# Performance work log

Measured on AMD Instinct MI355X. Metric: run time of the kernel, lower is better.

Reference implementation:

```python
import jax, jax.numpy as jnp
import numpy as np

M_USERS = 100000
N_ITEMS = 50000
N_NODES = M_USERS + N_ITEMS
DIM = 64
N_INTER = 1600000
BATCH = 16384
N_NEG = 40
REG = 1e-4


def setup_inputs() -> dict:
    key = jax.random.key(0)
    ks = jax.random.split(key, 12)
    xavier = lambda k, shape: jax.random.normal(k, shape, jnp.float32) * np.sqrt(2.0 / (shape[-1] + shape[-2] if len(shape) >= 2 else shape[-1] + 1))
    E = jax.random.normal(ks[0], (N_NODES, DIM), jnp.float32) * 0.1
    E2 = jax.random.normal(ks[1], (N_NODES, DIM), jnp.float32) * 0.1
    Wm = jax.random.normal(ks[2], (2, DIM, DIM), jnp.float32) * np.sqrt(1.0 / DIM)
    bm = jnp.zeros((2, DIM), jnp.float32)
    attn_W = jax.random.normal(ks[3], (DIM, DIM), jnp.float32) * np.sqrt(1.0 / DIM)
    attn_b = jnp.zeros((DIM,), jnp.float32)
    q_w = jax.random.normal(ks[4], (DIM,), jnp.float32) * np.sqrt(1.0 / DIM)
    # symmetric bipartite edge list: users in [0, M), items in [M, M+N)
    eu = jax.random.randint(ks[5], (N_INTER,), 0, M_USERS, jnp.int32)
    ei = jax.random.randint(ks[6], (N_INTER,), M_USERS, N_NODES, jnp.int32)
    edge_index = jnp.stack([jnp.concatenate([eu, ei]), jnp.concatenate([ei, eu])], axis=0)
    u = jax.random.randint(ks[7], (BATCH,), 0, M_USERS, jnp.int32)
    v = jax.random.randint(ks[8], (BATCH,), M_USERS, N_NODES, jnp.int32)
    n = jax.random.randint(ks[9], (BATCH, N_NEG), M_USERS, N_NODES, jnp.int32)
    w = jax.random.uniform(ks[10], (BATCH,), jnp.float32, 0.5, 5.0)  # ratings; only sign() used
    return {"E": E, "E2": E2, "Wm": Wm, "bm": bm, "attn_W": attn_W, "attn_b": attn_b,
            "q_w": q_w, "edge_index": edge_index, "u": u, "v": v, "n": n, "w": w}


def _lightgconv(x, src, dst, norm):
    # out[i] = sum_{(j->i)} norm_e * x[j]   (symmetric-normalized LightGCN propagate)
    msg = x[src] * norm[:, None]  # [E, D]
    return jax.ops.segment_sum(msg, dst, num_segments=N_NODES)


def _aggregate(E, E2, Wm, bm, attn_W, attn_b, q_w, edge_index):
    src, dst = edge_index[0], edge_index[1]
    deg = jax.ops.segment_sum(jnp.ones(src.shape, E.dtype), dst, num_segments=N_NODES)
    dinv = jnp.where(deg > 0, jax.lax.rsqrt(jnp.maximum(deg, 1.0)), 0.0)
    norm = dinv[src] * dinv[dst]
    # GNN branch: B = [E, conv(E), conv(conv(E))]; z_p = mean
    b1 = _lightgconv(E, src, dst, norm)
    b2 = _lightgconv(b1, src, dst, norm)
    z_p = (E + b1 + b2) / 3.0
    # MLP branch (eval mode: dropout disabled); z_n is output of last MLP layer
    x = jax.nn.relu(E2 @ Wm[0].T + bm[0])
    x = jax.nn.relu(x @ Wm[1].T + bm[1])
    z_n = x
    # attention fusion
    w_p = jnp.tanh(z_p @ attn_W.T + attn_b) @ q_w  # [Nn]
    w_n = jnp.tanh(z_n @ attn_W.T + attn_b) @ q_w  # [Nn]
    alpha = jax.nn.softmax(jnp.stack([w_p, w_n], axis=1), axis=1)  # [Nn, 2]
    return alpha[:, 0:1] * z_p + alpha[:, 1:2] * z_n


def reference(E, E2, Wm, bm, attn_W, attn_b, q_w, edge_index, u, v, n, w):
    Z = _aggregate(E, E2, Wm, bm, attn_W, attn_b, q_w, edge_index)
    u_ = Z[u]            # [B, D]
    v_ = Z[v]            # [B, D]
    n_ = Z[n]            # [B, K, D]
    pos = jnp.sum(u_ * v_, axis=1)                      # [B]
    neg = jnp.einsum('bd,bkd->bk', u_, n_)              # [B, K]
    sbpr = jax.nn.log_sigmoid(jnp.sign(w)[:, None] * pos[:, None] - neg).sum(axis=1)
    reg_loss = jnp.sum(u_ ** 2) + jnp.sum(v_ ** 2) + jnp.sum(n_ ** 2)
    return -jnp.sum(sbpr) + REG * reg_loss
```

## Files before the change

### kernel.cpp

```cpp
#include <hip/hip_runtime.h>
#include <math.h>


typedef unsigned int uint;
typedef unsigned short ushort;
typedef unsigned long long ull;
typedef __attribute__((ext_vector_type(8))) short short8v;
typedef __attribute__((ext_vector_type(4))) float float4v;
typedef __attribute__((ext_vector_type(2))) float float2v;

#define BK_SHIFT 9
#define BK_SIZE 512
#define CAP 20480

#if __has_builtin(__builtin_amdgcn_cvt_pk_f32_fp8) && __has_builtin(__builtin_amdgcn_cvt_pk_fp8_f32)
#define HW_FP8 1
#else
#define HW_FP8 0
#endif

__device__ inline float b2f(ushort u) { return __uint_as_float(((uint)u) << 16); }
__device__ inline ushort f2b(float f) {
  uint u = __float_as_uint(f);
  return (ushort)((u + 0x7fffu + ((u >> 16) & 1u)) >> 16);
}
__device__ inline uint pack2(float lo, float hi) {
  return (uint)f2b(lo) | ((uint)f2b(hi) << 16);
}

__device__ inline float dec1(uint u) {
  uint e = (u >> 3) & 0xFu;
  uint m = u & 7u;
  uint s = (u & 0x80u) << 24;
  float norm = __uint_as_float(s | ((e + 120u) << 23) | (m << 20));
  float den = __uint_as_float(s | 0x3F800000u) * (float)(int)m * 0.001953125f;
  return e ? norm : den;
}
__device__ inline uint enc1(float x) {
  uint s = (__float_as_uint(x) >> 24) & 0x80u;
  float ax = fminf(fabsf(x), 448.f);
  uint r;
  if (ax < 0.015625f) {
    r = (uint)(int)rintf(ax * 512.f);
  } else {
    uint b = __float_as_uint(ax);
    b += 0x7FFFFu + ((b >> 20) & 1u);
    uint e = (b >> 23) - 120u;
    r = (e > 15u) ? 0x7Eu : ((e << 3) | ((b >> 20) & 7u));
  }
  return s | r;
}
__device__ inline float4 dec4(uint v) {
#if HW_FP8
  float2v lo = __builtin_amdgcn_cvt_pk_f32_fp8((int)v, false);
  float2v hi = __builtin_amdgcn_cvt_pk_f32_fp8((int)v, true);
  return make_float4(lo[0], lo[1], hi[0], hi[1]);
#else
  return make_float4(dec1(v & 0xFFu), dec1((v >> 8) & 0xFFu),
                     dec1((v >> 16) & 0xFFu), dec1(v >> 24));
#endif
}
__device__ inline uint enc4f(float a, float b, float c, float d) {
#if HW_FP8
  int v = 0;
  v = __builtin_amdgcn_cvt_pk_fp8_f32(a, b, v, false);
  v = __builtin_amdgcn_cvt_pk_fp8_f32(c, d, v, true);
  return (uint)v;
#else
  return enc1(a) | (enc1(b) << 8) | (enc1(c) << 16) | (enc1(d) << 24);
#endif
}

__global__ void k_half(const float* __restrict__ x, ushort* __restrict__ out, int n8) {
  int i = blockIdx.x * blockDim.x + threadIdx.x;
  if (i >= n8) return;
  const float4* p = (const float4*)(x + (size_t)i * 8);
  float4 a = p[0], b = p[1];
  uint4 o;
  o.x = pack2(a.x, a.y); o.y = pack2(a.z, a.w);
  o.z = pack2(b.x, b.y); o.w = pack2(b.z, b.w);
  ((uint4*)out)[i] = o;
}

__global__ void k_conv_e(const float* __restrict__ x, uint* __restrict__ out8,
                         ushort* __restrict__ outh, int n16) {
  int i = blockIdx.x * blockDim.x + threadIdx.x;
  if (i >= n16) return;
  const float4* p = (const float4*)(x + (size_t)i * 16);
  float4 f0 = p[0], f1 = p[1], f2 = p[2], f3 = p[3];
  uint4 o8;
  o8.x = enc4f(f0.x, f0.y, f0.z, f0.w);
  o8.y = enc4f(f1.x, f1.y, f1.z, f1.w);
  o8.z = enc4f(f2.x, f2.y, f2.z, f2.w);
  o8.w = enc4f(f3.x, f3.y, f3.z, f3.w);
  ((uint4*)out8)[i] = o8;
  uint4 h0, h1;
  h0.x = pack2(f0.x, f0.y); h0.y = pack2(f0.z, f0.w);
  h0.z = pack2(f1.x, f1.y); h0.w = pack2(f1.z, f1.w);
  h1.x = pack2(f2.x, f2.y); h1.y = pack2(f2.z, f2.w);
  h1.z = pack2(f3.x, f3.y); h1.w = pack2(f3.z, f3.w);
  ((uint4*)outh)[2 * i] = h0;
  ((uint4*)outh)[2 * i + 1] = h1;
}

__global__ __launch_bounds__(512) void k_bucket(const int* __restrict__ src,
                                                const int* __restrict__ dst,
                                                int* __restrict__ gcursor,
                                                ull* __restrict__ ebuf,
                                                int NE, int nbkt, int chunk) {
  __shared__ int hist[1024];
  __shared__ int curb[1024];
  int tid = threadIdx.x;
  int nt = blockDim.x;
  for (int g = tid; g < nbkt; g += nt) hist[g] = 0;
  __syncthreads();
  int lo = blockIdx.x * chunk;
  int hi = min(lo + chunk, NE);
  for (int e = lo + tid; e < hi; e += nt)
    atomicAdd(&hist[dst[e] >> BK_SHIFT], 1);
  __syncthreads();
  for (int g = tid; g < nbkt; g += nt) {
    int c = hist[g];
    curb[g] = (c > 0) ? atomicAdd(&gcursor[g], c) : 0;
  }
  __syncthreads();
  for (int e = lo + tid; e < hi; e += nt) {
    int d = dst[e];
    int g = d >> BK_SHIFT;
    int pos = atomicAdd(&curb[g], 1);
    if (pos < CAP)
      ebuf[(size_t)g * CAP + pos] = ((ull)(uint)(d & (BK_SIZE - 1)) << 32) | (uint)src[e];
  }
}

__global__ void k_small(const int* __restrict__ gcursor, int* __restrict__ bktbase,
                        int nbkt) {
  __shared__ int sm[1024];
  int t = threadIdx.x;
  int v = (t < nbkt) ? gcursor[t] : 0;
  sm[t] = v;
  __syncthreads();
  for (int off = 1; off < 1024; off <<= 1) {
    int a = (t >= off) ? sm[t - off] : 0;
    __syncthreads();
    sm[t] += a;
    __syncthreads();
  }
  if (t < nbkt) bktbase[t] = sm[t] - v;
  if (t == 0) bktbase[nbkt] = sm[1023];
}

__global__ __launch_bounds__(256) void k_fine(const ull* __restrict__ ebuf,
                                              const int* __restrict__ gcursor,
                                              const int* __restrict__ bktbase,
                                              int* __restrict__ rowptr,
                                              float* __restrict__ dinv,
                                              int* __restrict__ csrc,
                                              int NN, int nbkt) {
  __shared__ int degl[BK_SIZE];
  __shared__ int lpl[BK_SIZE];
  __shared__ int ssum[256];
  int g = blockIdx.x;
  int tid = threadIdx.x;
  int cnt = gcursor[g];
  int base = bktbase[g];
  size_t ebase = (size_t)g * CAP;
  for (int j = tid; j < BK_SIZE; j += 256) degl[j] = 0;
  __syncthreads();
  for (int i = tid; i < cnt; i += 256)
    atomicAdd(&degl[(int)(ebuf[ebase + i] >> 32)], 1);
  __syncthreads();
  int d0 = degl[2 * tid], d1 = degl[2 * tid + 1];
  int s = d0 + d1;
  ssum[tid] = s;
  __syncthreads();
  for (int off = 1; off < 256; off <<= 1) {
    int a = (tid >= off) ? ssum[tid - off] : 0;
    __syncthreads();
    ssum[tid] += a;
    __syncthreads();
  }
  int excl = ssum[tid] - s;
  lpl[2 * tid] = excl;
  lpl[2 * tid + 1] = excl + d0;
  int node0 = g * BK_SIZE;
  int n0 = node0 + 2 * tid, n1 = n0 + 1;
  if (n0 < NN) {
    rowptr[n0] = base + excl;
    dinv[n0] = (d0 > 0) ? rsqrtf((float)d0) : 0.f;
  }
  if (n1 < NN) {
    rowptr[n1] = base + excl + d0;
    dinv[n1] = (d1 > 0) ? rsqrtf((float)d1) : 0.f;
  }
  if (g == nbkt - 1 && tid == 255) rowptr[NN] = base + excl + d0 + d1;
  __syncthreads();
  for (int i = tid; i < cnt; i += 256) {
    ull e = ebuf[ebase + i];
    int dl = (int)(e >> 32);
    int r = atomicAdd(&lpl[dl], 1);
    csrc[base + r] = (int)(uint)e;
  }
}

__global__ __launch_bounds__(256) void k_gather(const uint* __restrict__ x,
                                                const int* __restrict__ rowptr,
                                                const int* __restrict__ csrc,
                                                const float* __restrict__ dinv,
                                                uint* __restrict__ out, int NN) {
  int gid = blockIdx.x * blockDim.x + threadIdx.x;
  int node = gid >> 4;
  if (node >= NN) return;
  int sl = gid & 15;
  int beg = rowptr[node], end = rowptr[node + 1];
  float dn = dinv[node];
  float a0 = 0.f, a1 = 0.f, a2 = 0.f, a3 = 0.f;
  float b0 = 0.f, b1 = 0.f, b2 = 0.f, b3 = 0.f;
  int i = beg;
  for (; i + 7 < end; i += 8) {
    int s0 = csrc[i], s1 = csrc[i + 1], s2 = csrc[i + 2], s3 = csrc[i + 3];
    int s4 = csrc[i + 4], s5 = csrc[i + 5], s6 = csrc[i + 6], s7 = csrc[i + 7];
    float n0 = dinv[s0], n1 = dinv[s1], n2 = dinv[s2], n3 = dinv[s3];
    float n4 = dinv[s4], n5 = dinv[s5], n6 = dinv[s6], n7 = dinv[s7];
    uint r0 = x[(size_t)s0 * 16 + sl];
    uint r1 = x[(size_t)s1 * 16 + sl];
    uint r2 = x[(size_t)s2 * 16 + sl];
    uint r3 = x[(size_t)s3 * 16 + sl];
    uint r4 = x[(size_t)s4 * 16 + sl];
    uint r5 = x[(size_t)s5 * 16 + sl];
    uint r6 = x[(size_t)s6 * 16 + sl];
    uint r7 = x[(size_t)s7 * 16 + sl];
    float4 d0 = dec4(r0), d1 = dec4(r1), d2 = dec4(r2), d3 = dec4(r3);
    float4 d4 = dec4(r4), d5 = dec4(r5), d6 = dec4(r6), d7 = dec4(r7);
    a0 += n0 * d0.x; a1 += n0 * d0.y; a2 += n0 * d0.z; a3 += n0 * d0.w;
    a0 += n1 * d1.x; a1 += n1 * d1.y; a2 += n1 * d1.z; a3 += n1 * d1.w;
    a0 += n2 * d2.x; a1 += n2 * d2.y; a2 += n2 * d2.z; a3 += n2 * d2.w;
    a0 += n3 * d3.x; a1 += n3 * d3.y; a2 += n3 * d3.z; a3 += n3 * d3.w;
    b0 += n4 * d4.x; b1 += n4 * d4.y; b2 += n4 * d4.z; b3 += n4 * d4.w;
    b0 += n5 * d5.x; b1 += n5 * d5.y; b2 += n5 * d5.z; b3 += n5 * d5.w;
    b0 += n6 * d6.x; b1 += n6 * d6.y; b2 += n6 * d6.z; b3 += n6 * d6.w;
    b0 += n7 * d7.x; b1 += n7 * d7.y; b2 += n7 * d7.z; b3 += n7 * d7.w;
  }
  for (; i < end; ++i) {
    int s0 = csrc[i];
    float n0 = dinv[s0];
    float4 d0 = dec4(x[(size_t)s0 * 16 + sl]);
    a0 += n0 * d0.x; a1 += n0 * d0.y; a2 += n0 * d0.z; a3 += n0 * d0.w;
  }
  a0 += b0; a1 += b1; a2 += b2; a3 += b3;
  out[(size_t)node * 16 + sl] = enc4f(a0 * dn, a1 * dn, a2 * dn, a3 * dn);
}

__device__ inline float fast_tanh(float x) {
  float t = __expf(fminf(fmaxf(2.f * x, -30.f), 30.f));
  return (t - 1.f) / (t + 1.f);
}

#define MFMA(a, b, c) __builtin_amdgcn_mfma_f32_16x16x32_bf16((a), (b), (c), 0, 0, 0)

__global__ __launch_bounds__(256, 2) void k_node(const ushort* __restrict__ Ebf,
                                                 const ushort* __restrict__ E2h,
                                                 const ushort* __restrict__ Wmh,
                                                 const float* __restrict__ bm,
                                                 const ushort* __restrict__ AWh,
                                                 const float* __restrict__ ab,
                                                 const float* __restrict__ qw,
                                                 const uint* __restrict__ b1q,
                                                 const uint* __restrict__ b2q,
                                                 ushort* __restrict__ Zh,
                                                 int NN) {
  __shared__ ushort Hl[64 * 72];
  __shared__ ushort Pl[64 * 72];
  int tid = threadIdx.x;
  int lane = tid & 63, wid = tid >> 6;
  int r15 = lane & 15, kg = lane >> 4;
  int node0 = blockIdx.x * 64;

  int arow = node0 + 16 * wid + r15;
  int arowc = min(arow, NN - 1);
  const ushort* e2p = E2h + (size_t)arowc * 64 + 8 * kg;
  short8v a0 = *(const short8v*)e2p;
  short8v a1 = *(const short8v*)(e2p + 32);
  float4v acc[4];
#pragma unroll
  for (int b = 0; b < 4; ++b) {
    int col = r15 + 16 * b;
    short8v w0 = *(const short8v*)&Wmh[col * 64 + 8 * kg];
    short8v w1 = *(const short8v*)&Wmh[col * 64 + 32 + 8 * kg];
    float bias = bm[col];
    acc[b] = (float4v){bias, bias, bias, bias};
    acc[b] = MFMA(a0, w0, acc[b]);
    acc[b] = MFMA(a1, w1, acc[b]);
  }
#pragma unroll
  for (int b = 0; b < 4; ++b)
#pragma unroll
    for (int rr = 0; rr < 4; ++rr)
      Hl[(16 * wid + 4 * kg + rr) * 72 + 16 * b + r15] = f2b(fmaxf(acc[b][rr], 0.f));

  {
    int row = tid >> 2;
    int c4 = (tid & 3) * 4;
    int node = node0 + row;
    uint outp[8];
    if (node < NN) {
      const ushort* pe = Ebf + (size_t)node * 64 + c4 * 4;
      uint4 eh0 = *(const uint4*)pe;
      uint4 eh1 = *(const uint4*)(pe + 8);
      uint4 q1 = *(const uint4*)(b1q + (size_t)node * 16 + c4);
      uint4 q2 = *(const uint4*)(b2q + (size_t)node * 16 + c4);
      float4 d1[4] = {dec4(q1.x), dec4(q1.y), dec4(q1.z), dec4(q1.w)};
      float4 d2[4] = {dec4(q2.x), dec4(q2.y), dec4(q2.z), dec4(q2.w)};
      const uint* ehw = (const uint*)&eh0;
      uint ehall[8] = {eh0.x, eh0.y, eh0.z, eh0.w, eh1.x, eh1.y, eh1.z, eh1.w};
      (void)ehw;
#pragma unroll
      for (int c = 0; c < 4; ++c) {
        float e0 = b2f((ushort)(ehall[2 * c] & 0xFFFFu));
        float e1 = b2f((ushort)(ehall[2 * c] >> 16));
        float e2 = b2f((ushort)(ehall[2 * c + 1] & 0xFFFFu));
        float e3 = b2f((ushort)(ehall[2 * c + 1] >> 16));
        float z0 = (e0 + d1[c].x + d2[c].x) * (1.f / 3.f);
        float z1 = (e1 + d1[c].y + d2[c].y) * (1.f / 3.f);
        float z2 = (e2 + d1[c].z + d2[c].z) * (1.f / 3.f);
        float z3 = (e3 + d1[c].w + d2[c].w) * (1.f / 3.f);
        outp[2 * c] = pack2(z0, z1);
        outp[2 * c + 1] = pack2(z2, z3);
      }
    } else {
#pragma unroll
      for (int c = 0; c < 8; ++c) outp[c] = 0;
    }
    int c0 = c4 * 4;
    *(uint4*)&Pl[row * 72 + c0] = *(uint4*)&outp[0];
    *(uint4*)&Pl[row * 72 + c0 + 8] = *(uint4*)&outp[4];
  }
  __syncthreads();

  const ushort* hap = &Hl[(16 * wid + r15) * 72 + 8 * kg];
  short8v ha0 = *(const short8v*)hap;
  short8v ha1 = *(const short8v*)(hap + 32);
  float4v acc2[4];
#pragma unroll
  for (int b = 0; b < 4; ++b) {
    int col = r15 + 16 * b;
    short8v w0 = *(const short8v*)&Wmh[4096 + col * 64 + 8 * kg];
    short8v w1 = *(const short8v*)&Wmh[4096 + col * 64 + 32 + 8 * kg];
    float bias = bm[64 + col];
    acc2[b] = (float4v){bias, bias, bias, bias};
    acc2[b] = MFMA(ha0, w0, acc2[b]);
    acc2[b] = MFMA(ha1, w1, acc2[b]);
  }
  __syncthreads();
#pragma unroll
  for (int b = 0; b < 4; ++b)
#pragma unroll
    for (int rr = 0; rr < 4; ++rr)
      Hl[(16 * wid + 4 * kg + rr) * 72 + 16 * b + r15] = f2b(fmaxf(acc2[b][rr], 0.f));
  __syncthreads();

  const ushort* pap = &Pl[(16 * wid + r15) * 72 + 8 * kg];
  short8v pa0 = *(const short8v*)pap;
  short8v pa1 = *(const short8v*)(pap + 32);
  const ushort* nap = &Hl[(16 * wid + r15) * 72 + 8 * kg];
  short8v na0 = *(const short8v*)nap;
  short8v na1 = *(const short8v*)(nap + 32);
  float4v ac1[4], ac2[4];
#pragma unroll
  for (int b = 0; b < 4; ++b) {
    int col = r15 + 16 * b;
    short8v w0 = *(const short8v*)&AWh[col * 64 + 8 * kg];
    short8v w1 = *(const short8v*)&AWh[col * 64 + 32 + 8 * kg];
    float bias = ab[col];
    ac1[b] = (float4v){bias, bias, bias, bias};
    ac1[b] = MFMA(pa0, w0, ac1[b]);
    ac1[b] = MFMA(pa1, w1, ac1[b]);
    ac2[b] = (float4v){bias, bias, bias, bias};
    ac2[b] = MFMA(na0, w0, ac2[b]);
    ac2[b] = MFMA(na1, w1, ac2[b]);
  }

  float qv[4];
#pragma unroll
  for (int b = 0; b < 4; ++b) qv[b] = qw[r15 + 16 * b];
#pragma unroll
  for (int rr = 0; rr < 4; ++rr) {
    float wp = 0.f, wn = 0.f;
#pragma unroll
    for (int b = 0; b < 4; ++b) {
      wp += fast_tanh(ac1[b][rr]) * qv[b];
      wn += fast_tanh(ac2[b][rr]) * qv[b];
    }
#pragma unroll
    for (int off = 8; off; off >>= 1) {
      wp += __shfl_xor(wp, off);
      wn += __shfl_xor(wn, off);
    }
    float m = fmaxf(wp, wn);
    float e1 = __expf(wp - m), e2 = __expf(wn - m);
    float inv = 1.f / (e1 + e2);
    float al0 = e1 * inv, al1 = e2 * inv;
    int row_l = 16 * wid + 4 * kg + rr;
    int node = node0 + row_l;
    if (node < NN) {
      ushort* op = Zh + (size_t)node * 64;
#pragma unroll
      for (int b = 0; b < 4; ++b) {
        int col = r15 + 16 * b;
        int li = row_l * 72 + col;
        op[col] = f2b(al0 * b2f(Pl[li]) + al1 * b2f(Hl[li]));
      }
    }
  }
}

__global__ __launch_bounds__(256) void k_score(const ushort* __restrict__ Z,
                                               const int* __restrict__ u,
                                               const int* __restrict__ v,
                                               const int* __restrict__ n,
                                               const float* __restrict__ w,
                                               float* __restrict__ out, int B, int K) {
  __shared__ float xbuf[16][65];
  __shared__ float part[16];
  int t = threadIdx.x;
  int wv = t >> 6, lane = t & 63;
  int sg = lane >> 4, sl = lane & 15;
  int bloc = wv * 4 + sg;
  int b = blockIdx.x * 16 + bloc;
  float lossb = 0.f;
  if (b < B) {
    int uid = u[b], vid = v[b];
    ushort4 uh = *(const ushort4*)&Z[(size_t)uid * 64 + sl * 4];
    ushort4 vh = *(const ushort4*)&Z[(size_t)vid * 64 + sl * 4];
    float ux = b2f(uh.x), uy = b2f(uh.y), uz = b2f(uh.z), uw = b2f(uh.w);
    float vx = b2f(vh.x), vy = b2f(vh.y), vz = b2f(vh.z), vw = b2f(vh.w);
    float p = ux * vx + uy * vy + uz * vz + uw * vw;
#pragma unroll
    for (int off = 8; off; off >>= 1) p += __shfl_xor(p, off);
    float wb = w[b];
    float sgn = (wb > 0.f) ? 1.f : ((wb < 0.f) ? -1.f : 0.f);
    float sp = sgn * p;
    float regl = ux * ux + uy * uy + uz * uz + uw * uw
               + vx * vx + vy * vy + vz * vz + vw * vw;
    const int* nb_ = n + (size_t)b * K;
    for (int k = 0; k < K; ++k) {
      int nid = nb_[k];
      ushort4 nh = *(const ushort4*)&Z[(size_t)nid * 64 + sl * 4];
      float nx = b2f(nh.x), ny = b2f(nh.y), nz = b2f(nh.z), nw = b2f(nh.w);
      float d = ux * nx + uy * ny + uz * nz + uw * nw;
      regl += nx * nx + ny * ny + nz * nz + nw * nw;
#pragma unroll
      for (int off = 8; off; off >>= 1) d += __shfl_xor(d, off);
      if (sl == 0) xbuf[bloc][k] = sp - d;
    }
#pragma unroll
    for (int off = 8; off; off >>= 1) regl += __shfl_xor(regl, off);
    float sb = 0.f;
    for (int k = sl; k < K; k += 16) {
      float x = xbuf[bloc][k];
      sb += fminf(x, 0.f) - log1pf(expf(-fabsf(x)));
    }
#pragma unroll
    for (int off = 8; off; off >>= 1) sb += __shfl_xor(sb, off);
    lossb = -sb + 1e-4f * regl;
  }
  if (sl == 0) part[bloc] = (b < B) ? lossb : 0.f;
  __syncthreads();
  if (t == 0) {
    float s = 0.f;
#pragma unroll
    for (int i = 0; i < 16; ++i) s += part[i];
    unsafeAtomicAdd(out, s);
  }
}

extern "C" void kernel_launch(void* const* d_in, const int* in_sizes, int n_in,
                              void* d_out, int out_size, void* d_ws, size_t ws_size,
                              hipStream_t stream) {
  const float* E  = (const float*)d_in[0];
  const float* E2 = (const float*)d_in[1];
  const float* Wm = (const float*)d_in[2];
  const float* bm = (const float*)d_in[3];
  const float* AW = (const float*)d_in[4];
  const float* ab = (const float*)d_in[5];
  const float* qw = (const float*)d_in[6];
  const int*   ei = (const int*)d_in[7];
  const int*   u  = (const int*)d_in[8];
  const int*   v  = (const int*)d_in[9];
  const int*   nn = (const int*)d_in[10];
  const float* w  = (const float*)d_in[11];

  const int NN = in_sizes[0] / 64;
  const int NE = in_sizes[7] / 2;
  const int B  = in_sizes[8];
  const int K  = in_sizes[10] / B;
  const int NBKT = (NN + BK_SIZE - 1) / BK_SIZE;

  const int* src = ei;
  const int* dst = ei + NE;

  float*  ws      = (float*)d_ws;
  float*  dinv    = ws;
  uint*   E8      = (uint*)(dinv + NN);
  uint*   b1q     = E8 + (size_t)NN * 16;
  uint*   b2q     = b1q + (size_t)NN * 16;
  ushort* E2h     = (ushort*)(b2q + (size_t)NN * 16);
  ushort* Wmh     = E2h + (size_t)NN * 64;
  ushort* AWh     = Wmh + 8192;
  int*    rowptr  = (int*)(AWh + 4096);
  int*    csrc    = rowptr + NN + 1;
  int*    gcursor = csrc + NE;
  int*    bktbase = gcursor + NBKT;
  ull*    ebuf    = (ull*)(((uintptr_t)(bktbase + NBKT + 1) + 15) & ~(uintptr_t)15);
  ushort* Zh      = (ushort*)ebuf;
  ushort* Ebf     = Zh + (size_t)NN * 64;
  float*  outf    = (float*)d_out;

  hipMemsetAsync(gcursor, 0, (size_t)NBKT * sizeof(int), stream);
  hipMemsetAsync(outf, 0, sizeof(float), stream);

  const int BUCKET_BLOCKS = 512;
  int chunk = (NE + BUCKET_BLOCKS - 1) / BUCKET_BLOCKS;
  k_bucket<<<BUCKET_BLOCKS, 512, 0, stream>>>(src, dst, gcursor, ebuf, NE, NBKT, chunk);
  k_small<<<1, 1024, 0, stream>>>(gcursor, bktbase, NBKT);
  k_fine<<<NBKT, 256, 0, stream>>>(ebuf, gcursor, bktbase, rowptr, dinv, csrc, NN, NBKT);

  k_conv_e<<<(NN * 4 + 255) / 256, 256, 0, stream>>>(E, E8, Ebf, NN * 4);
  k_half<<<(NN * 8 + 255) / 256, 256, 0, stream>>>(E2, E2h, NN * 8);
  k_half<<<4, 256, 0, stream>>>(Wm, Wmh, 1024);
  k_half<<<2, 256, 0, stream>>>(AW, AWh, 512);

  int gatherBlocks = ((size_t)NN * 16 + 255) / 256;
  k_gather<<<gatherBlocks, 256, 0, stream>>>(E8, rowptr, csrc, dinv, b1q, NN);
  k_gather<<<gatherBlocks, 256, 0, stream>>>(b1q, rowptr, csrc, dinv, b2q, NN);

  int nodeTiles = (NN + 63) / 64;
  k_node<<<nodeTiles, 256, 0, stream>>>(Ebf, E2h, Wmh, bm, AWh, ab, qw, b1q, b2q, Zh, NN);

  k_score<<<(B + 15) / 16, 256, 0, stream>>>(Zh, u, v, nn, w, outf, B, K);
}
```

Measured before the change: 303.6 us.

## Pre-scale gather sources by dinv and fuse conversion kernels

The source-side normalization dinv[src] is folded into the stored fp8 features: E is scaled by dinv when converted, and the first gather writes a second copy of its output scaled by dinv squared. The gather kernels no longer do a random dinv[src] load and multiply per edge. The E, E2 and weight conversion kernels are merged into two launches. In exchange there are extra fp8 writes and an extra NN*64-byte workspace buffer. Quantizing pre-scaled values changes where fp8 rounding error lands, and the gather unroll drops from 8 to 4, which reduces memory-level parallelism.

```diff
diff --git a/kernel.cpp b/kernel.cpp
--- a/kernel.cpp
+++ b/kernel.cpp
@@ -71,36 +71,53 @@
 #endif
 }
 
-__global__ void k_half(const float* __restrict__ x, ushort* __restrict__ out, int n8) {
+__global__ void k_conv(const float* __restrict__ E, const float* __restrict__ E2,
+                       const float* __restrict__ dinv,
+                       uint* __restrict__ E8s, ushort* __restrict__ Ebf,
+                       ushort* __restrict__ E2h, int n4) {
   int i = blockIdx.x * blockDim.x + threadIdx.x;
-  if (i >= n8) return;
-  const float4* p = (const float4*)(x + (size_t)i * 8);
-  float4 a = p[0], b = p[1];
-  uint4 o;
-  o.x = pack2(a.x, a.y); o.y = pack2(a.z, a.w);
-  o.z = pack2(b.x, b.y); o.w = pack2(b.z, b.w);
-  ((uint4*)out)[i] = o;
-}
-
-__global__ void k_conv_e(const float* __restrict__ x, uint* __restrict__ out8,
-                         ushort* __restrict__ outh, int n16) {
-  int i = blockIdx.x * blockDim.x + threadIdx.x;
-  if (i >= n16) return;
-  const float4* p = (const float4*)(x + (size_t)i * 16);
-  float4 f0 = p[0], f1 = p[1], f2 = p[2], f3 = p[3];
+  if (i >= n4) return;
+  int node = i >> 2;
+  float dn = dinv[node];
+  const float4* pe = (const float4*)(E + (size_t)i * 16);
+  float4 f0 = pe[0], f1 = pe[1], f2 = pe[2], f3 = pe[3];
   uint4 o8;
-  o8.x = enc4f(f0.x, f0.y, f0.z, f0.w);
-  o8.y = enc4f(f1.x, f1.y, f1.z, f1.w);
-  o8.z = enc4f(f2.x, f2.y, f2.z, f2.w);
-  o8.w = enc4f(f3.x, f3.y, f3.z, f3.w);
-  ((uint4*)out8)[i] = o8;
+  o8.x = enc4f(dn * f0.x, dn * f0.y, dn * f0.z, dn * f0.w);
+  o8.y = enc4f(dn * f1.x, dn * f1.y, dn * f1.z, dn * f1.w);
+  o8.z = enc4f(dn * f2.x, dn * f2.y, dn * f2.z, dn * f2.w);
+  o8.w = enc4f(dn * f3.x, dn * f3.y, dn * f3.z, dn * f3.w);
+  ((uint4*)E8s)[i] = o8;
   uint4 h0, h1;
   h0.x = pack2(f0.x, f0.y); h0.y = pack2(f0.z, f0.w);
   h0.z = pack2(f1.x, f1.y); h0.w = pack2(f1.z, f1.w);
   h1.x = pack2(f2.x, f2.y); h1.y = pack2(f2.z, f2.w);
   h1.z = pack2(f3.x, f3.y); h1.w = pack2(f3.z, f3.w);
-  ((uint4*)outh)[2 * i] = h0;
-  ((uint4*)outh)[2 * i + 1] = h1;
+  ((uint4*)Ebf)[2 * i] = h0;
+  ((uint4*)Ebf)[2 * i + 1] = h1;
+  const float4* p2 = (const float4*)(E2 + (size_t)i * 16);
+  float4 g0 = p2[0], g1 = p2[1], g2 = p2[2], g3 = p2[3];
+  uint4 e0, e1;
+  e0.x = pack2(g0.x, g0.y); e0.y = pack2(g0.z, g0.w);
+  e0.z = pack2(g1.x, g1.y); e0.w = pack2(g1.z, g1.w);
+  e1.x = pack2(g2.x, g2.y); e1.y = pack2(g2.z, g2.w);
+  e1.z = pack2(g3.x, g3.y); e1.w = pack2(g3.z, g3.w);
+  ((uint4*)E2h)[2 * i] = e0;
+  ((uint4*)E2h)[2 * i + 1] = e1;
+}
+
+__global__ void k_convw(const float* __restrict__ Wm, const float* __restrict__ AW,
+                        ushort* __restrict__ Wmh, ushort* __restrict__ AWh) {
+  int i = blockIdx.x * blockDim.x + threadIdx.x;
+  const float* srcp;
+  ushort* dstp;
+  if (i < 1024) { srcp = Wm + (size_t)i * 8; dstp = Wmh + (size_t)i * 8; }
+  else if (i < 1536) { srcp = AW + (size_t)(i - 1024) * 8; dstp = AWh + (size_t)(i - 1024) * 8; }
+  else return;
+  float4 a = ((const float4*)srcp)[0], b = ((const float4*)srcp)[1];
+  uint4 o;
+  o.x = pack2(a.x, a.y); o.y = pack2(a.z, a.w);
+  o.z = pack2(b.x, b.y); o.w = pack2(b.z, b.w);
+  *(uint4*)dstp = o;
 }
 
 __global__ __launch_bounds__(512) void k_bucket(const int* __restrict__ src,
@@ -207,7 +224,8 @@
                                                 const int* __restrict__ rowptr,
                                                 const int* __restrict__ csrc,
                                                 const float* __restrict__ dinv,
-                                                uint* __restrict__ out, int NN) {
+                                                uint* __restrict__ out1,
+                                                uint* __restrict__ outs, int NN) {
   int gid = blockIdx.x * blockDim.x + threadIdx.x;
   int node = gid >> 4;
   if (node >= NN) return;
@@ -215,40 +233,28 @@
   int beg = rowptr[node], end = rowptr[node + 1];
   float dn = dinv[node];
   float a0 = 0.f, a1 = 0.f, a2 = 0.f, a3 = 0.f;
-  float b0 = 0.f, b1 = 0.f, b2 = 0.f, b3 = 0.f;
   int i = beg;
-  for (; i + 7 < end; i += 8) {
+  for (; i + 3 < end; i += 4) {
     int s0 = csrc[i], s1 = csrc[i + 1], s2 = csrc[i + 2], s3 = csrc[i + 3];
-    int s4 = csrc[i + 4], s5 = csrc[i + 5], s6 = csrc[i + 6], s7 = csrc[i + 7];
-    float n0 = dinv[s0], n1 = dinv[s1], n2 = dinv[s2], n3 = dinv[s3];
-    float n4 = dinv[s4], n5 = dinv[s5], n6 = dinv[s6], n7 = dinv[s7];
     uint r0 = x[(size_t)s0 * 16 + sl];
     uint r1 = x[(size_t)s1 * 16 + sl];
     uint r2 = x[(size_t)s2 * 16 + sl];
     uint r3 = x[(size_t)s3 * 16 + sl];
-    uint r4 = x[(size_t)s4 * 16 + sl];
-    uint r5 = x[(size_t)s5 * 16 + sl];
-    uint r6 = x[(size_t)s6 * 16 + sl];
-    uint r7 = x[(size_t)s7 * 16 + sl];
     float4 d0 = dec4(r0), d1 = dec4(r1), d2 = dec4(r2), d3 = dec4(r3);
-    float4 d4 = dec4(r4), d5 = dec4(r5), d6 = dec4(r6), d7 = dec4(r7);
-    a0 += n0 * d0.x; a1 += n0 * d0.y; a2 += n0 * d0.z; a3 += n0 * d0.w;
-    a0 += n1 * d1.x; a1 += n1 * d1.y; a2 += n1 * d1.z; a3 += n1 * d1.w;
-    a0 += n2 * d2.x; a1 += n2 * d2.y; a2 += n2 * d2.z; a3 += n2 * d2.w;
-    a0 += n3 * d3.x; a1 += n3 * d3.y; a2 += n3 * d3.z; a3 += n3 * d3.w;
-    b0 += n4 * d4.x; b1 += n4 * d4.y; b2 += n4 * d4.z; b3 += n4 * d4.w;
-    b0 += n5 * d5.x; b1 += n5 * d5.y; b2 += n5 * d5.z; b3 += n5 * d5.w;
-    b0 += n6 * d6.x; b1 += n6 * d6.y; b2 += n6 * d6.z; b3 += n6 * d6.w;
-    b0 += n7 * d7.x; b1 += n7 * d7.y; b2 += n7 * d7.z; b3 += n7 * d7.w;
+    a0 += d0.x + d1.x + d2.x + d3.x;
+    a1 += d0.y + d1.y + d2.y + d3.y;
+    a2 += d0.z + d1.z + d2.z + d3.z;
+    a3 += d0.w + d1.w + d2.w + d3.w;
   }
   for (; i < end; ++i) {
-    int s0 = csrc[i];
-    float n0 = dinv[s0];
-    float4 d0 = dec4(x[(size_t)s0 * 16 + sl]);
-    a0 += n0 * d0.x; a1 += n0 * d0.y; a2 += n0 * d0.z; a3 += n0 * d0.w;
-  }
-  a0 += b0; a1 += b1; a2 += b2; a3 += b3;
-  out[(size_t)node * 16 + sl] = enc4f(a0 * dn, a1 * dn, a2 * dn, a3 * dn);
+    float4 d0 = dec4(x[(size_t)csrc[i] * 16 + sl]);
+    a0 += d0.x; a1 += d0.y; a2 += d0.z; a3 += d0.w;
+  }
+  out1[(size_t)node * 16 + sl] = enc4f(a0 * dn, a1 * dn, a2 * dn, a3 * dn);
+  if (outs) {
+    float dn2 = dn * dn;
+    outs[(size_t)node * 16 + sl] = enc4f(a0 * dn2, a1 * dn2, a2 * dn2, a3 * dn2);
+  }
 }
 
 __device__ inline float fast_tanh(float x) {
@@ -311,9 +317,7 @@
       uint4 q2 = *(const uint4*)(b2q + (size_t)node * 16 + c4);
       float4 d1[4] = {dec4(q1.x), dec4(q1.y), dec4(q1.z), dec4(q1.w)};
       float4 d2[4] = {dec4(q2.x), dec4(q2.y), dec4(q2.z), dec4(q2.w)};
-      const uint* ehw = (const uint*)&eh0;
       uint ehall[8] = {eh0.x, eh0.y, eh0.z, eh0.w, eh1.x, eh1.y, eh1.z, eh1.w};
-      (void)ehw;
 #pragma unroll
       for (int c = 0; c < 4; ++c) {
         float e0 = b2f((ushort)(ehall[2 * c] & 0xFFFFu));
@@ -501,9 +505,10 @@
 
   float*  ws      = (float*)d_ws;
   float*  dinv    = ws;
-  uint*   E8      = (uint*)(dinv + NN);
-  uint*   b1q     = E8 + (size_t)NN * 16;
-  uint*   b2q     = b1q + (size_t)NN * 16;
+  uint*   E8s     = (uint*)(dinv + NN);
+  uint*   b1q     = E8s + (size_t)NN * 16;
+  uint*   b1s     = b1q + (size_t)NN * 16;
+  uint*   b2q     = b1s + (size_t)NN * 16;
   ushort* E2h     = (ushort*)(b2q + (size_t)NN * 16);
   ushort* Wmh     = E2h + (size_t)NN * 64;
   ushort* AWh     = Wmh + 8192;
@@ -525,14 +530,12 @@
   k_small<<<1, 1024, 0, stream>>>(gcursor, bktbase, NBKT);
   k_fine<<<NBKT, 256, 0, stream>>>(ebuf, gcursor, bktbase, rowptr, dinv, csrc, NN, NBKT);
 
-  k_conv_e<<<(NN * 4 + 255) / 256, 256, 0, stream>>>(E, E8, Ebf, NN * 4);
-  k_half<<<(NN * 8 + 255) / 256, 256, 0, stream>>>(E2, E2h, NN * 8);
-  k_half<<<4, 256, 0, stream>>>(Wm, Wmh, 1024);
-  k_half<<<2, 256, 0, stream>>>(AW, AWh, 512);
+  k_conv<<<(NN * 4 + 255) / 256, 256, 0, stream>>>(E, E2, dinv, E8s, Ebf, E2h, NN * 4);
+  k_convw<<<6, 256, 0, stream>>>(Wm, AW, Wmh, AWh);
 
   int gatherBlocks = ((size_t)NN * 16 + 255) / 256;
-  k_gather<<<gatherBlocks, 256, 0, stream>>>(E8, rowptr, csrc, dinv, b1q, NN);
-  k_gather<<<gatherBlocks, 256, 0, stream>>>(b1q, rowptr, csrc, dinv, b2q, NN);
+  k_gather<<<gatherBlocks, 256, 0, stream>>>(E8s, rowptr, csrc, dinv, b1q, b1s, NN);
+  k_gather<<<gatherBlocks, 256, 0, stream>>>(b1s, rowptr, csrc, dinv, b2q, (uint*)nullptr, NN);
 
   int nodeTiles = (NN + 63) / 64;
   k_node<<<nodeTiles, 256, 0, stream>>>(Ebf, E2h, Wmh, bm, AWh, ab, qw, b1q, b2q, Zh, NN);
```

New measurement: 282.8 us. 6.8% less time.
